# Kernel optimization log

Hardware: AMD Instinct MI355X
Metric: run time of the kernel (lower is better)

Reference implementation:

```python
import jax, jax.numpy as jnp
import numpy as np

IMG = 224                      # hardcoded image_size in apply_mask
K = int(0.25 * IMG * IMG)      # 12544 pixels masked per sample


def setup_inputs() -> dict:
    key = jax.random.key(0)
    k1, k2 = jax.random.split(key)
    B = 256
    data = jax.random.normal(k1, (B, IMG, IMG, 3), dtype=jnp.float32)
    # |gradients| flattened over (H, W, C) -> length IMG*IMG*3, nonnegative
    line_grad = jax.random.uniform(k2, (B, IMG * IMG * 3), dtype=jnp.float32)
    return {"data": data, "line_grad": line_grad}


def _mask_one(d, g):
    # d: [IMG, IMG, 3], g: [IMG*IMG*3]
    _, idx = jax.lax.top_k(g, K)              # flat indices into (H,W,C)
    reduced = jnp.mod(idx, IMG * IMG)         # fold channel offset -> spatial
    rows = reduced // IMG
    cols = reduced % IMG
    # scatter zeros across all 3 channels at the selected pixels
    return d.at[rows, cols].set(0.0)


def reference(data, line_grad):
    # vectorized_map over the batch -> vmap
    return jax.vmap(_mask_one)(data, line_grad)
```

## Files before the change

kernel.cpp:

```cpp
#include <hip/hip_runtime.h>

#define IMG    224
#define NPIX   (IMG * IMG)
#define NELEM  (NPIX * 3)
#define KSEL   12544
#define NBINS  4096
#define NVEC4  (NELEM / 4)

#define K1_CHUNKS 4
#define K1_BLOCK  256
#define K1_V4     (NVEC4 / K1_CHUNKS)

#define CH        8
#define PIX_PER   (NPIX / CH)
#define QUADS_PER (PIX_PER / 4)
#define MWORDS    (PIX_PER / 32)
#define EV4_PER   (PIX_PER * 3 / 4)

#define CAP 512

__global__ __launch_bounds__(K1_BLOCK) void k1_hist(
    const float* __restrict__ grad, unsigned int* __restrict__ hist)
{
    const int s     = blockIdx.x >> 2;
    const int chunk = blockIdx.x & 3;
    const float4* g4 = (const float4*)(grad + (size_t)s * NELEM);

    __shared__ unsigned int h[NBINS];
    for (int i = threadIdx.x; i < NBINS; i += K1_BLOCK) h[i] = 0u;
    __syncthreads();

    const int beg = chunk * K1_V4, end = beg + K1_V4;
    for (int i = beg + threadIdx.x; i < end; i += K1_BLOCK) {
        float4 v = g4[i];
        atomicAdd(&h[min((int)(v.x * 4096.0f), NBINS - 1)], 1u);
        atomicAdd(&h[min((int)(v.y * 4096.0f), NBINS - 1)], 1u);
        atomicAdd(&h[min((int)(v.z * 4096.0f), NBINS - 1)], 1u);
        atomicAdd(&h[min((int)(v.w * 4096.0f), NBINS - 1)], 1u);
    }
    __syncthreads();

    unsigned int* gh = hist + (size_t)s * NBINS;
    for (int i = threadIdx.x; i < NBINS; i += K1_BLOCK)
        if (h[i]) atomicAdd(&gh[i], h[i]);
}

__global__ __launch_bounds__(1024) void k2_scan(
    const unsigned int* __restrict__ hist,
    uint2* __restrict__ thr, unsigned int* __restrict__ candcnt)
{
    const int s   = blockIdx.x;
    const int tid = threadIdx.x;
    const unsigned int* h = hist + (size_t)s * NBINS;

    unsigned int h0 = h[4 * tid], h1 = h[4 * tid + 1];
    unsigned int h2 = h[4 * tid + 2], h3 = h[4 * tid + 3];
    const unsigned int gsum = h0 + h1 + h2 + h3;

    const int lane = tid & 63, w = tid >> 6;
    unsigned int v = gsum;
    #pragma unroll
    for (int off = 1; off < 64; off <<= 1) {
        unsigned int u = __shfl_down(v, off, 64);
        if (lane + off < 64) v += u;
    }
    __shared__ unsigned int wtot[16];
    if (lane == 0) wtot[w] = v;
    __syncthreads();
    unsigned int tail = 0;
    for (int i = w + 1; i < 16; ++i) tail += wtot[i];

    const unsigned int suffix     = v + tail;
    const unsigned int suffixNext = suffix - gsum;

    if (suffix >= KSEL && suffixNext < KSEL) {
        unsigned int cum = suffixNext;
        unsigned int hh[4] = {h0, h1, h2, h3};
        for (int i = 3; i >= 0; --i) {
            cum += hh[i];
            if (cum >= KSEL) {
                thr[s] = make_uint2((unsigned)(4 * tid + i),
                                    (unsigned)(KSEL - (cum - hh[i])));
                break;
            }
        }
    }
    if (tid == 0) candcnt[s] = 0u;
}

__global__ __launch_bounds__(256) void k3_apply(
    const float* __restrict__ data, const float* __restrict__ grad,
    const uint2* __restrict__ thr,
    unsigned int* __restrict__ candcnt,
    unsigned int* __restrict__ candkey, unsigned int* __restrict__ candidx,
    float* __restrict__ out)
{
    const int s     = blockIdx.x >> 3;
    const int chunk = blockIdx.x & 7;
    const int p0    = chunk * PIX_PER;

    const uint2 t  = thr[s];
    const float t0 = (float)t.x * (1.0f / 4096.0f);
    const float t1 = (float)(t.x + 1) * (1.0f / 4096.0f);

    __shared__ unsigned int mask[MWORDS];
    for (int i = threadIdx.x; i < MWORDS; i += 256) mask[i] = 0u;
    __syncthreads();

    const float4* g4 = (const float4*)(grad + (size_t)s * NELEM);
    unsigned int* ck = candkey + (size_t)s * CAP;
    unsigned int* ci = candidx + (size_t)s * CAP;

    for (int q = threadIdx.x; q < QUADS_PER; q += 256) {
        const int p = p0 + 4 * q;
        float4 a = g4[p >> 2];
        float4 b = g4[(p + NPIX) >> 2];
        float4 c = g4[(p + 2 * NPIX) >> 2];
        float av[4] = {a.x, a.y, a.z, a.w};
        float bv[4] = {b.x, b.y, b.z, b.w};
        float cv[4] = {c.x, c.y, c.z, c.w};
        unsigned int m = 0;
        #pragma unroll
        for (int j = 0; j < 4; ++j) {
            if ((av[j] >= t1) || (bv[j] >= t1) || (cv[j] >= t1)) m |= (1u << j);
            if (av[j] >= t0 && av[j] < t1) {
                unsigned int cc = atomicAdd(&candcnt[s], 1u);
                if (cc < CAP) { ck[cc] = __float_as_uint(av[j]); ci[cc] = (unsigned)(p + j); }
            }
            if (bv[j] >= t0 && bv[j] < t1) {
                unsigned int cc = atomicAdd(&candcnt[s], 1u);
                if (cc < CAP) { ck[cc] = __float_as_uint(bv[j]); ci[cc] = (unsigned)(NPIX + p + j); }
            }
            if (cv[j] >= t0 && cv[j] < t1) {
                unsigned int cc = atomicAdd(&candcnt[s], 1u);
                if (cc < CAP) { ck[cc] = __float_as_uint(cv[j]); ci[cc] = (unsigned)(2 * NPIX + p + j); }
            }
        }
        if (m) atomicOr(&mask[q >> 3], m << ((4 * q) & 31));
    }
    __syncthreads();

    const float4* d4 = (const float4*)(data + (size_t)s * NELEM + (size_t)3 * p0);
    float4*       o4 = (float4*)(out  + (size_t)s * NELEM + (size_t)3 * p0);
    for (int i = threadIdx.x; i < EV4_PER; i += 256) {
        float4 v = d4[i];
        const int e = 4 * i;
        const int lp0 = e / 3, lp1 = (e + 1) / 3, lp2 = (e + 2) / 3, lp3 = (e + 3) / 3;
        if ((mask[lp0 >> 5] >> (lp0 & 31)) & 1u) v.x = 0.0f;
        if ((mask[lp1 >> 5] >> (lp1 & 31)) & 1u) v.y = 0.0f;
        if ((mask[lp2 >> 5] >> (lp2 & 31)) & 1u) v.z = 0.0f;
        if ((mask[lp3 >> 5] >> (lp3 & 31)) & 1u) v.w = 0.0f;
        o4[i] = v;
    }
}

__global__ __launch_bounds__(64) void k4_ties(
    const uint2* __restrict__ thr, const unsigned int* __restrict__ candcnt,
    const unsigned int* __restrict__ candkey, const unsigned int* __restrict__ candidx,
    float* __restrict__ out)
{
    const int s = blockIdx.x;
    const unsigned int n = min(candcnt[s], (unsigned int)CAP);
    const unsigned int r = thr[s].y;
    const unsigned int* ck = candkey + (size_t)s * CAP;
    const unsigned int* ci = candidx + (size_t)s * CAP;

    __shared__ unsigned int k_[CAP], i_[CAP];
    for (unsigned int i = threadIdx.x; i < n; i += 64) { k_[i] = ck[i]; i_[i] = ci[i]; }
    __syncthreads();

    float* o = out + (size_t)s * NELEM;
    for (unsigned int j = threadIdx.x; j < n; j += 64) {
        const unsigned int kj = k_[j], ij = i_[j];
        unsigned int rank = 0;
        for (unsigned int i = 0; i < n; ++i)
            rank += (k_[i] > kj) || (k_[i] == kj && i_[i] < ij);
        if (rank < r) {
            const int p = (int)(ij % NPIX);
            o[3 * p] = 0.0f; o[3 * p + 1] = 0.0f; o[3 * p + 2] = 0.0f;
        }
    }
}

#define MAXCAND 2048
#define NMASKW (NPIX / 32)
#define BLOCK  1024

__global__ __launch_bounds__(BLOCK) void masked_model_kernel(
    const float* __restrict__ data,
    const float* __restrict__ grad,
    float* __restrict__ out)
{
    const int b   = blockIdx.x;
    const int tid = threadIdx.x;

    const float* g = grad + (size_t)b * NELEM;
    const float* d = data + (size_t)b * NELEM;
    float*       o = out  + (size_t)b * NELEM;

    __shared__ unsigned int hist[NBINS];
    __shared__ unsigned int suffixP[BLOCK + 1];
    __shared__ unsigned int mask[NMASKW];
    __shared__ unsigned int candkey[MAXCAND];
    __shared__ unsigned int candidx[MAXCAND];
    __shared__ unsigned int candcnt;
    __shared__ int sB1;
    __shared__ unsigned int sR;

    for (int i = tid; i < NBINS; i += BLOCK) hist[i] = 0u;
    for (int i = tid; i < NMASKW; i += BLOCK) mask[i] = 0u;
    if (tid == 0) { candcnt = 0u; suffixP[BLOCK] = 0u; }
    __syncthreads();

    const float4* g4 = (const float4*)g;
    for (int i = tid; i < NVEC4; i += BLOCK) {
        float4 v = g4[i];
        atomicAdd(&hist[min((int)(v.x * 4096.0f), NBINS - 1)], 1u);
        atomicAdd(&hist[min((int)(v.y * 4096.0f), NBINS - 1)], 1u);
        atomicAdd(&hist[min((int)(v.z * 4096.0f), NBINS - 1)], 1u);
        atomicAdd(&hist[min((int)(v.w * 4096.0f), NBINS - 1)], 1u);
    }
    __syncthreads();

    {
        unsigned int sv = hist[4 * tid] + hist[4 * tid + 1]
                        + hist[4 * tid + 2] + hist[4 * tid + 3];
        suffixP[tid] = sv;
        __syncthreads();
        for (int off = 1; off < BLOCK; off <<= 1) {
            unsigned int v = suffixP[tid];
            if (tid + off < BLOCK) v += suffixP[tid + off];
            __syncthreads();
            suffixP[tid] = v;
            __syncthreads();
        }
    }
    {
        unsigned int a  = suffixP[tid];
        unsigned int nx = suffixP[tid + 1];
        if (a >= KSEL && nx < KSEL) {
            unsigned int cum = nx;
            for (int i = 3; i >= 0; --i) {
                unsigned int h = hist[4 * tid + i];
                cum += h;
                if (cum >= KSEL) { sB1 = 4 * tid + i; sR = KSEL - (cum - h); break; }
            }
        }
    }
    __syncthreads();

    {
        const int B1 = sB1;
        for (int i = tid; i < NVEC4; i += BLOCK) {
            float4 v = g4[i];
            int base = 4 * i;
            float vv[4] = {v.x, v.y, v.z, v.w};
            #pragma unroll
            for (int c = 0; c < 4; ++c) {
                int bin = min((int)(vv[c] * 4096.0f), NBINS - 1);
                if (bin > B1) {
                    int p = (base + c) % NPIX;
                    atomicOr(&mask[p >> 5], 1u << (p & 31));
                } else if (bin == B1) {
                    unsigned int c2 = atomicAdd(&candcnt, 1u);
                    if (c2 < MAXCAND) {
                        candkey[c2] = __float_as_uint(vv[c]);
                        candidx[c2] = (unsigned int)(base + c);
                    }
                }
            }
        }
    }
    __syncthreads();

    {
        unsigned int n = candcnt < MAXCAND ? candcnt : MAXCAND;
        unsigned int r = sR;
        for (unsigned int j = tid; j < n; j += BLOCK) {
            unsigned int kj = candkey[j];
            unsigned int ij = candidx[j];
            unsigned int rank = 0;
            for (unsigned int i = 0; i < n; ++i) {
                unsigned int ki = candkey[i];
                rank += (ki > kj) || (ki == kj && candidx[i] < ij);
            }
            if (rank < r) {
                int p = (int)(ij % NPIX);
                atomicOr(&mask[p >> 5], 1u << (p & 31));
            }
        }
    }
    __syncthreads();

    {
        const float4* d4 = (const float4*)d;
        float4*       o4 = (float4*)o;
        for (int i = tid; i < NVEC4; i += BLOCK) {
            float4 v = d4[i];
            int e = 4 * i;
            int p0 = e / 3, p1 = (e + 1) / 3, p2 = (e + 2) / 3, p3 = (e + 3) / 3;
            if ((mask[p0 >> 5] >> (p0 & 31)) & 1u) v.x = 0.0f;
            if ((mask[p1 >> 5] >> (p1 & 31)) & 1u) v.y = 0.0f;
            if ((mask[p2 >> 5] >> (p2 & 31)) & 1u) v.z = 0.0f;
            if ((mask[p3 >> 5] >> (p3 & 31)) & 1u) v.w = 0.0f;
            o4[i] = v;
        }
    }
}

extern "C" void kernel_launch(void* const* d_in, const int* in_sizes, int n_in,
                              void* d_out, int out_size, void* d_ws, size_t ws_size,
                              hipStream_t stream) {
    const float* data = (const float*)d_in[0];
    const float* grad = (const float*)d_in[1];
    float* out = (float*)d_out;

    const int B = in_sizes[0] / NELEM;

    const size_t histB = (size_t)B * NBINS * sizeof(unsigned int);
    const size_t thrB  = (size_t)B * sizeof(uint2);
    const size_t cntB  = (size_t)B * sizeof(unsigned int);
    const size_t cntPad = (cntB + 7) & ~(size_t)7;
    const size_t keyB  = (size_t)B * CAP * sizeof(unsigned int);

    char* p = (char*)d_ws;
    unsigned int* hist = (unsigned int*)p;  p += histB;
    uint2*        thr  = (uint2*)p;         p += thrB;
    unsigned int* cnt  = (unsigned int*)p;  p += cntPad;
    unsigned int* ckey = (unsigned int*)p;  p += keyB;
    unsigned int* cidx = (unsigned int*)p;  p += keyB;
    const size_t need = (size_t)(p - (char*)d_ws);

    if (ws_size >= need) {
        hipMemsetAsync(hist, 0, histB, stream);
        k1_hist<<<B * K1_CHUNKS, K1_BLOCK, 0, stream>>>(grad, hist);
        k2_scan<<<B, 1024, 0, stream>>>(hist, thr, cnt);
        k3_apply<<<B * CH, 256, 0, stream>>>(data, grad, thr, cnt, ckey, cidx, out);
        k4_ties<<<B, 64, 0, stream>>>(thr, cnt, ckey, cidx, out);
    } else {
        masked_model_kernel<<<B, BLOCK, 0, stream>>>(data, grad, out);
    }
}
```

Before: 397.3 us.

## Write per-chunk sub-histograms, build mask via shuffles, vectorize masked copy

The histogram kernel now writes each chunk's shared histogram to its own slice of global memory with plain vector stores. This removes the global atomics and the memset launch, and the scan kernel sums the four sub-histograms on load. The apply kernel builds the candidate and mask bits with branchless compares and combines 4-bit masks across 8 lanes with xor-shuffles before one plain store, replacing the shared-memory atomicOr and its zero-init pass. The output pass handles a pixel quad (three float4s) per iteration, which drops the per-element divide-by-3. The cost is more workspace and more histogram traffic into the scan kernel.

```diff
diff --git a/kernel.cpp b/kernel.cpp
--- a/kernel.cpp
+++ b/kernel.cpp
@@ -15,12 +15,11 @@
 #define PIX_PER   (NPIX / CH)
 #define QUADS_PER (PIX_PER / 4)
 #define MWORDS    (PIX_PER / 32)
-#define EV4_PER   (PIX_PER * 3 / 4)
 
 #define CAP 512
 
 __global__ __launch_bounds__(K1_BLOCK) void k1_hist(
-    const float* __restrict__ grad, unsigned int* __restrict__ hist)
+    const float* __restrict__ grad, unsigned int* __restrict__ subhist)
 {
     const int s     = blockIdx.x >> 2;
     const int chunk = blockIdx.x & 3;
@@ -40,21 +39,27 @@
     }
     __syncthreads();
 
-    unsigned int* gh = hist + (size_t)s * NBINS;
-    for (int i = threadIdx.x; i < NBINS; i += K1_BLOCK)
-        if (h[i]) atomicAdd(&gh[i], h[i]);
+    uint4* dst = (uint4*)(subhist + ((size_t)s * K1_CHUNKS + chunk) * NBINS);
+    const uint4* hv = (const uint4*)h;
+    for (int i = threadIdx.x; i < NBINS / 4; i += K1_BLOCK) dst[i] = hv[i];
 }
 
 __global__ __launch_bounds__(1024) void k2_scan(
-    const unsigned int* __restrict__ hist,
+    const unsigned int* __restrict__ subhist,
     uint2* __restrict__ thr, unsigned int* __restrict__ candcnt)
 {
     const int s   = blockIdx.x;
     const int tid = threadIdx.x;
-    const unsigned int* h = hist + (size_t)s * NBINS;
-
-    unsigned int h0 = h[4 * tid], h1 = h[4 * tid + 1];
-    unsigned int h2 = h[4 * tid + 2], h3 = h[4 * tid + 3];
+    const uint4* sh = (const uint4*)(subhist + (size_t)s * K1_CHUNKS * NBINS);
+
+    uint4 a0 = sh[tid];
+    uint4 a1 = sh[1024 + tid];
+    uint4 a2 = sh[2048 + tid];
+    uint4 a3 = sh[3072 + tid];
+    const unsigned int h0 = a0.x + a1.x + a2.x + a3.x;
+    const unsigned int h1 = a0.y + a1.y + a2.y + a3.y;
+    const unsigned int h2 = a0.z + a1.z + a2.z + a3.z;
+    const unsigned int h3 = a0.w + a1.w + a2.w + a3.w;
     const unsigned int gsum = h0 + h1 + h2 + h3;
 
     const int lane = tid & 63, w = tid >> 6;
@@ -98,14 +103,13 @@
     const int s     = blockIdx.x >> 3;
     const int chunk = blockIdx.x & 7;
     const int p0    = chunk * PIX_PER;
+    const int lane  = threadIdx.x & 63;
 
     const uint2 t  = thr[s];
     const float t0 = (float)t.x * (1.0f / 4096.0f);
     const float t1 = (float)(t.x + 1) * (1.0f / 4096.0f);
 
     __shared__ unsigned int mask[MWORDS];
-    for (int i = threadIdx.x; i < MWORDS; i += 256) mask[i] = 0u;
-    __syncthreads();
 
     const float4* g4 = (const float4*)(grad + (size_t)s * NELEM);
     unsigned int* ck = candkey + (size_t)s * CAP;
@@ -116,41 +120,62 @@
         float4 a = g4[p >> 2];
         float4 b = g4[(p + NPIX) >> 2];
         float4 c = g4[(p + 2 * NPIX) >> 2];
-        float av[4] = {a.x, a.y, a.z, a.w};
-        float bv[4] = {b.x, b.y, b.z, b.w};
-        float cv[4] = {c.x, c.y, c.z, c.w};
-        unsigned int m = 0;
-        #pragma unroll
-        for (int j = 0; j < 4; ++j) {
-            if ((av[j] >= t1) || (bv[j] >= t1) || (cv[j] >= t1)) m |= (1u << j);
-            if (av[j] >= t0 && av[j] < t1) {
-                unsigned int cc = atomicAdd(&candcnt[s], 1u);
-                if (cc < CAP) { ck[cc] = __float_as_uint(av[j]); ci[cc] = (unsigned)(p + j); }
-            }
-            if (bv[j] >= t0 && bv[j] < t1) {
-                unsigned int cc = atomicAdd(&candcnt[s], 1u);
-                if (cc < CAP) { ck[cc] = __float_as_uint(bv[j]); ci[cc] = (unsigned)(NPIX + p + j); }
-            }
-            if (cv[j] >= t0 && cv[j] < t1) {
-                unsigned int cc = atomicAdd(&candcnt[s], 1u);
-                if (cc < CAP) { ck[cc] = __float_as_uint(cv[j]); ci[cc] = (unsigned)(2 * NPIX + p + j); }
-            }
-        }
-        if (m) atomicOr(&mask[q >> 3], m << ((4 * q) & 31));
+
+        unsigned int s1 = 0, s0 = 0;
+        s1 |= (a.x >= t1) << 0;  s1 |= (a.y >= t1) << 1;
+        s1 |= (a.z >= t1) << 2;  s1 |= (a.w >= t1) << 3;
+        s1 |= (b.x >= t1) << 4;  s1 |= (b.y >= t1) << 5;
+        s1 |= (b.z >= t1) << 6;  s1 |= (b.w >= t1) << 7;
+        s1 |= (c.x >= t1) << 8;  s1 |= (c.y >= t1) << 9;
+        s1 |= (c.z >= t1) << 10; s1 |= (c.w >= t1) << 11;
+        s0 |= (a.x >= t0) << 0;  s0 |= (a.y >= t0) << 1;
+        s0 |= (a.z >= t0) << 2;  s0 |= (a.w >= t0) << 3;
+        s0 |= (b.x >= t0) << 4;  s0 |= (b.y >= t0) << 5;
+        s0 |= (b.z >= t0) << 6;  s0 |= (b.w >= t0) << 7;
+        s0 |= (c.x >= t0) << 8;  s0 |= (c.y >= t0) << 9;
+        s0 |= (c.z >= t0) << 10; s0 |= (c.w >= t0) << 11;
+
+        unsigned int m = (s1 | (s1 >> 4) | (s1 >> 8)) & 0xFu;
+
+        unsigned int wword = m << (4 * (lane & 7));
+        wword |= __shfl_xor(wword, 1, 64);
+        wword |= __shfl_xor(wword, 2, 64);
+        wword |= __shfl_xor(wword, 4, 64);
+        if ((lane & 7) == 0) mask[q >> 3] = wword;
+
+        unsigned int candm = s0 & ~s1;
+        if (candm) {
+            do {
+                const int j  = __ffs(candm) - 1;
+                candm &= candm - 1;
+                const int pl = j >> 2, e = j & 3;
+                const float4 src = (pl == 0) ? a : (pl == 1) ? b : c;
+                const float val = (e == 0) ? src.x : (e == 1) ? src.y
+                                : (e == 2) ? src.z : src.w;
+                const unsigned int cc = atomicAdd(&candcnt[s], 1u);
+                if (cc < CAP) {
+                    ck[cc] = __float_as_uint(val);
+                    ci[cc] = (unsigned int)(pl * NPIX + p + e);
+                }
+            } while (candm);
+        }
     }
     __syncthreads();
 
     const float4* d4 = (const float4*)(data + (size_t)s * NELEM + (size_t)3 * p0);
     float4*       o4 = (float4*)(out  + (size_t)s * NELEM + (size_t)3 * p0);
-    for (int i = threadIdx.x; i < EV4_PER; i += 256) {
-        float4 v = d4[i];
-        const int e = 4 * i;
-        const int lp0 = e / 3, lp1 = (e + 1) / 3, lp2 = (e + 2) / 3, lp3 = (e + 3) / 3;
-        if ((mask[lp0 >> 5] >> (lp0 & 31)) & 1u) v.x = 0.0f;
-        if ((mask[lp1 >> 5] >> (lp1 & 31)) & 1u) v.y = 0.0f;
-        if ((mask[lp2 >> 5] >> (lp2 & 31)) & 1u) v.z = 0.0f;
-        if ((mask[lp3 >> 5] >> (lp3 & 31)) & 1u) v.w = 0.0f;
-        o4[i] = v;
+    for (int q = threadIdx.x; q < QUADS_PER; q += 256) {
+        const unsigned int bits = (mask[q >> 3] >> (4 * (q & 7))) & 0xFu;
+        float4 v0 = d4[3 * q];
+        float4 v1 = d4[3 * q + 1];
+        float4 v2 = d4[3 * q + 2];
+        if (bits & 1u) { v0.x = 0.0f; v0.y = 0.0f; v0.z = 0.0f; }
+        if (bits & 2u) { v0.w = 0.0f; v1.x = 0.0f; v1.y = 0.0f; }
+        if (bits & 4u) { v1.z = 0.0f; v1.w = 0.0f; v2.x = 0.0f; }
+        if (bits & 8u) { v2.y = 0.0f; v2.z = 0.0f; v2.w = 0.0f; }
+        o4[3 * q]     = v0;
+        o4[3 * q + 1] = v1;
+        o4[3 * q + 2] = v2;
     }
 }
 
@@ -317,24 +342,23 @@
 
     const int B = in_sizes[0] / NELEM;
 
-    const size_t histB = (size_t)B * NBINS * sizeof(unsigned int);
-    const size_t thrB  = (size_t)B * sizeof(uint2);
-    const size_t cntB  = (size_t)B * sizeof(unsigned int);
+    const size_t subB = (size_t)B * K1_CHUNKS * NBINS * sizeof(unsigned int);
+    const size_t thrB = (size_t)B * sizeof(uint2);
+    const size_t cntB = (size_t)B * sizeof(unsigned int);
     const size_t cntPad = (cntB + 7) & ~(size_t)7;
-    const size_t keyB  = (size_t)B * CAP * sizeof(unsigned int);
+    const size_t keyB = (size_t)B * CAP * sizeof(unsigned int);
 
     char* p = (char*)d_ws;
-    unsigned int* hist = (unsigned int*)p;  p += histB;
-    uint2*        thr  = (uint2*)p;         p += thrB;
-    unsigned int* cnt  = (unsigned int*)p;  p += cntPad;
-    unsigned int* ckey = (unsigned int*)p;  p += keyB;
-    unsigned int* cidx = (unsigned int*)p;  p += keyB;
+    unsigned int* subhist = (unsigned int*)p;  p += subB;
+    uint2*        thr     = (uint2*)p;         p += thrB;
+    unsigned int* cnt     = (unsigned int*)p;  p += cntPad;
+    unsigned int* ckey    = (unsigned int*)p;  p += keyB;
+    unsigned int* cidx    = (unsigned int*)p;  p += keyB;
     const size_t need = (size_t)(p - (char*)d_ws);
 
     if (ws_size >= need) {
-        hipMemsetAsync(hist, 0, histB, stream);
-        k1_hist<<<B * K1_CHUNKS, K1_BLOCK, 0, stream>>>(grad, hist);
-        k2_scan<<<B, 1024, 0, stream>>>(hist, thr, cnt);
+        k1_hist<<<B * K1_CHUNKS, K1_BLOCK, 0, stream>>>(grad, subhist);
+        k2_scan<<<B, 1024, 0, stream>>>(subhist, thr, cnt);
         k3_apply<<<B * CH, 256, 0, stream>>>(data, grad, thr, cnt, ckey, cidx, out);
         k4_ties<<<B, 64, 0, stream>>>(thr, cnt, ckey, cidx, out);
     } else {
```

After: 402.0 us. Within noise of the previous version (+1.2%).
